# Kernel optimization log

Measured on AMD Instinct MI355X. Metric: run time of the kernel, lower is better.

Reference implementation:

```python
import jax, jax.numpy as jnp
import numpy as np

B, L, D_IN = 4, 2048, 1024
D_KEY, D_VAL = 1024, 1024
N_SLOTS, TOPK = 32768, 16
TEMP = 0.1
EPS = 1e-5


def layer_norm(x, g, b):
    mu = jnp.mean(x, axis=-1, keepdims=True)
    var = jnp.var(x, axis=-1, keepdims=True)
    return (x - mu) * jax.lax.rsqrt(var + EPS) * g + b


def setup_inputs() -> dict:
    key = jax.random.key(0)
    ks = jax.random.split(key, 8)
    s_in = 1.0 / np.sqrt(D_IN)
    s_ft = 1.0 / np.sqrt(D_IN + D_VAL + 1)
    return {
        "h_in": jax.random.normal(ks[0], (B, L, D_IN), jnp.float32),
        "Wk": jax.random.normal(ks[1], (D_IN, D_KEY), jnp.float32) * s_in,
        "bk": jnp.zeros((D_KEY,), jnp.float32),
        "cube_keys": jax.random.normal(ks[2], (N_SLOTS, D_KEY), jnp.float32),
        "cube_vals": jax.random.normal(ks[3], (N_SLOTS, D_VAL), jnp.float32) * 0.1,
        "ln_in_g": jnp.ones((D_IN,), jnp.float32),
        "ln_in_b": jnp.zeros((D_IN,), jnp.float32),
        "ln_pred_g": jnp.ones((D_VAL,), jnp.float32),
        "ln_pred_b": jnp.zeros((D_VAL,), jnp.float32),
        "W1": jax.random.normal(ks[4], (D_IN + D_VAL + 1, D_IN), jnp.float32) * s_ft,
        "b1": jnp.zeros((D_IN,), jnp.float32),
        "W2": jax.random.normal(ks[5], (D_IN, 1), jnp.float32) * s_in,
        "b2": jnp.zeros((1,), jnp.float32),
    }


def reference(h_in, Wk, bk, cube_keys, cube_vals, ln_in_g, ln_in_b,
              ln_pred_g, ln_pred_b, W1, b1, W2, b2):
    Bv, Lv, Dv = h_in.shape
    # key projection -> [B*L, d_key]
    keys = (jnp.einsum('bld,dk->blk', h_in, Wk) + bk).reshape(Bv * Lv, -1)
    # cube kNN query: cosine similarity against slot keys
    kn = keys * jax.lax.rsqrt(jnp.sum(keys * keys, -1, keepdims=True) + 1e-8)
    mn = cube_keys * jax.lax.rsqrt(jnp.sum(cube_keys * cube_keys, -1, keepdims=True) + 1e-8)
    sims = kn @ mn.T                                   # [BL, N]
    top_sims, idx = jax.lax.top_k(sims, TOPK)          # [BL, K]
    w = jax.nn.softmax(top_sims / TEMP, axis=-1)       # retrieval weights
    vals = jnp.take(cube_vals, idx, axis=0)            # [BL, K, d_val] gather
    pred = jnp.einsum('nk,nkd->nd', w, vals).reshape(Bv, Lv, -1)
    conf = ((top_sims[:, 0] + 1.0) * 0.5).reshape(Bv, Lv, 1)
    # gate
    feats = jnp.concatenate([layer_norm(h_in, ln_in_g, ln_in_b),
                             layer_norm(pred, ln_pred_g, ln_pred_b),
                             conf], axis=-1)
    hmid = jax.nn.silu(jnp.einsum('blf,fd->bld', feats, W1) + b1)
    alpha = jnp.clip(jax.nn.sigmoid(jnp.einsum('bld,do->blo', hmid, W2) + b2), 0.0, 1.0)
    # blend (y_teacher is None): (1-a)*h + a*(h+pred)
    y_out = (1.0 - alpha) * h_in + alpha * (h_in + pred)
    return y_out, jnp.mean(alpha), jnp.mean(conf)
```

## Files before the change

kernel.cpp:

```cpp
#include <hip/hip_runtime.h>
#include <hip/hip_bf16.h>
#include <cstdint>
#include <cstddef>

typedef __bf16 bf16;
typedef __bf16 bf16x4 __attribute__((ext_vector_type(4)));
typedef __bf16 bf16x8 __attribute__((ext_vector_type(8)));
typedef float  f32x4  __attribute__((ext_vector_type(4)));

#define BL      8192
#define DDIM    1024
#define NSLOTS  32768
#define NSPLIT  8
#define SLOTS_PER (NSLOTS / NSPLIT)
#define CAP     49

#define WS_MN    ((size_t)0)
#define WS_PRED  ((size_t)0)
#define WS_HBF   ((size_t)67108864)
#define WS_HMID  WS_HBF
#define WS_WKT   ((size_t)83886080)
#define WS_W1T   ((size_t)85983232)
#define WS_KEYS  ((size_t)90177536)
#define WS_FEATS WS_KEYS
#define WS_KN    ((size_t)123731968)
#define WS_TPK   ((size_t)140509184)
#define WS_CONF  ((size_t)148897792)

__device__ __forceinline__ void async16(const void* g, void* l) {
  __builtin_amdgcn_global_load_lds(
      (const __attribute__((address_space(1))) void*)g,
      (__attribute__((address_space(3))) void*)(uintptr_t)(uint32_t)(uintptr_t)l,
      16, 0, 0);
}

__device__ __forceinline__ void stage_tile(const bf16* __restrict__ src, int ld,
                                           bf16* lds, int tid) {
  const int wave = tid >> 6;
#pragma unroll
  for (int issue = 0; issue < 2; ++issue) {
    const int gi  = issue * 256 + tid;
    const int row = gi >> 2;
    const int gc  = gi & 3;
    const bf16* g = src + (size_t)row * ld + gc * 8;
    bf16* l = lds + (size_t)(issue * 256 + wave * 64) * 8;
    async16(g, l);
  }
}

__device__ __forceinline__ f32x4 mfma_bf16(bf16x8 a, bf16x8 b, f32x4 c) {
  return __builtin_amdgcn_mfma_f32_16x16x32_bf16(a, b, c, 0, 0, 0);
}

__device__ __forceinline__ float block_sum(float v, float* red) {
#pragma unroll
  for (int off = 32; off > 0; off >>= 1) v += __shfl_xor(v, off, 64);
  const int tid = threadIdx.x;
  if ((tid & 63) == 0) red[tid >> 6] = v;
  __syncthreads();
  v = red[0] + red[1] + red[2] + red[3];
  __syncthreads();
  return v;
}

__device__ __forceinline__ uint32_t pack_key(float v, int slot) {
  return ((__float_as_uint(v) ^ 0x80000000u) & 0xFFFF8000u) | (uint32_t)slot;
}

__device__ __forceinline__ void drain_merge(uint32_t* cand, int* cnt, int rb_own,
                                            uint32_t (&tk)[16], float& thrF) {
  int n = cnt[rb_own];
  n = n > CAP ? CAP : n;
  for (int t = 0;; ++t) {
    if (!__any(t < n)) break;
    uint32_t cur = 0u;
    if (t < n) cur = cand[rb_own * CAP + t];
#pragma unroll
    for (int p = 0; p < 16; ++p) {
      const uint32_t old = tk[p];
      const uint32_t mx = old > cur ? old : cur;
      tk[p] = mx;
      cur = old > cur ? cur : old;
    }
  }
  cnt[rb_own] = 0;
  thrF = __uint_as_float((tk[15] & 0xFFFF8000u) ^ 0x80000000u);
}

__global__ void cvt_bf16_kernel(const float* __restrict__ in, bf16* __restrict__ out, int n4) {
  int i = blockIdx.x * blockDim.x + threadIdx.x;
  if (i >= n4) return;
  f32x4 v = *(const f32x4*)(in + (size_t)i * 4);
  bf16x4 o = {(bf16)v.x, (bf16)v.y, (bf16)v.z, (bf16)v.w};
  *(bf16x4*)(out + (size_t)i * 4) = o;
}

__global__ void transpose_f32_bf16(const float* __restrict__ in, bf16* __restrict__ out,
                                   int R, int C) {
  __shared__ float tile[32][33];
  const int c0 = blockIdx.x * 32, r0 = blockIdx.y * 32;
  for (int i = threadIdx.y; i < 32; i += 8)
    tile[i][threadIdx.x] = in[(size_t)(r0 + i) * C + c0 + threadIdx.x];
  __syncthreads();
  for (int i = threadIdx.y; i < 32; i += 8)
    out[(size_t)(c0 + i) * R + r0 + threadIdx.x] = (bf16)tile[threadIdx.x][i];
}

__global__ __launch_bounds__(256) void rownorm_kernel(const float* __restrict__ in,
                                                      bf16* __restrict__ out) {
  __shared__ float red[4];
  const int row = blockIdx.x, t = threadIdx.x;
  f32x4 v = *(const f32x4*)(in + (size_t)row * 1024 + t * 4);
  float sq = v.x * v.x + v.y * v.y + v.z * v.z + v.w * v.w;
  sq = block_sum(sq, red);
  float sc = rsqrtf(sq + 1e-8f);
  bf16x4 o = {(bf16)(v.x * sc), (bf16)(v.y * sc), (bf16)(v.z * sc), (bf16)(v.w * sc)};
  *(bf16x4*)(out + (size_t)row * 1024 + t * 4) = o;
}

template <int EPI>
__global__ __launch_bounds__(256, 2) void gemm_bt_kernel(
    const bf16* __restrict__ A, const bf16* __restrict__ Bm, int Kd,
    float* __restrict__ Cf, bf16* __restrict__ Cb,
    const float* __restrict__ bias, const float* __restrict__ conf,
    const float* __restrict__ w1c) {
  __shared__ bf16 As[128 * 32];
  __shared__ bf16 Bs[128 * 32];
  const int tid = threadIdx.x;
  const int lane = tid & 63, wave = tid >> 6;
  const int wr = (wave >> 1) * 64, wc = (wave & 1) * 64;
  const int m0 = blockIdx.x * 128, n0 = blockIdx.y * 128;
  const int ar = lane & 15, ak = (lane >> 4) * 8;

  f32x4 acc[4][4];
#pragma unroll
  for (int i = 0; i < 4; ++i)
#pragma unroll
    for (int j = 0; j < 4; ++j) acc[i][j] = (f32x4){0.f, 0.f, 0.f, 0.f};

  for (int k0 = 0; k0 < Kd; k0 += 32) {
    __syncthreads();
    stage_tile(A + (size_t)m0 * Kd + k0, Kd, As, tid);
    stage_tile(Bm + (size_t)n0 * Kd + k0, Kd, Bs, tid);
    __syncthreads();
    bf16x8 af[4], bfr[4];
#pragma unroll
    for (int i = 0; i < 4; ++i)
      af[i] = *(const bf16x8*)(As + (wr + i * 16 + ar) * 32 + ak);
#pragma unroll
    for (int j = 0; j < 4; ++j)
      bfr[j] = *(const bf16x8*)(Bs + (wc + j * 16 + ar) * 32 + ak);
#pragma unroll
    for (int i = 0; i < 4; ++i)
#pragma unroll
      for (int j = 0; j < 4; ++j)
        acc[i][j] = mfma_bf16(af[i], bfr[j], acc[i][j]);
  }

  const int mq = (lane >> 4) * 4, nq = lane & 15;
#pragma unroll
  for (int i = 0; i < 4; ++i)
#pragma unroll
    for (int j = 0; j < 4; ++j)
#pragma unroll
      for (int r = 0; r < 4; ++r) {
        const int m = m0 + wr + i * 16 + mq + r;
        const int n = n0 + wc + j * 16 + nq;
        float x = acc[i][j][r];
        if (EPI == 0) {
          Cf[(size_t)m * 1024 + n] = x + bias[n];
        } else {
          x += bias[n] + conf[m] * w1c[n];
          x = x / (1.f + expf(-x));
          Cb[(size_t)m * 1024 + n] = (bf16)x;
        }
      }
}

__global__ __launch_bounds__(256, 2) void sims_topk_kernel(
    const bf16* __restrict__ kn, const bf16* __restrict__ mn,
    uint32_t* __restrict__ tpk) {
  __shared__ bf16 As[128 * 32];
  __shared__ bf16 Bs0[128 * 32];
  __shared__ bf16 Bs1[128 * 32];
  __shared__ uint32_t cand[256 * CAP];
  __shared__ int cnt[256];

  const int tid = threadIdx.x;
  const int lane = tid & 63, wave = tid >> 6;
  const int wr = (wave >> 1) * 64;
  const int ch = wave & 1;
  const int split = blockIdx.x;
  const int m0 = blockIdx.y * 128;
  const int sbeg = split * SLOTS_PER;
  const int ar = lane & 15, ak = (lane >> 4) * 8;
  const int mq = (lane >> 4) * 4, nq = lane & 15;
  const int rb_own = (wr + lane) * 2 + ch;

  cnt[tid] = 0;

  uint32_t tk[16];
#pragma unroll
  for (int j = 0; j < 16; ++j) tk[j] = 0u;
  float thrF = __uint_as_float(0x80000000u);

  for (int it = 0; it < SLOTS_PER / 256; ++it) {
    f32x4 acc[2][4][4];
#pragma unroll
    for (int c = 0; c < 2; ++c)
#pragma unroll
      for (int i = 0; i < 4; ++i)
#pragma unroll
        for (int j = 0; j < 4; ++j) acc[c][i][j] = (f32x4){0.f, 0.f, 0.f, 0.f};

    const int n0 = sbeg + it * 256;
    for (int k0 = 0; k0 < 1024; k0 += 32) {
      __syncthreads();
      stage_tile(kn + (size_t)m0 * 1024 + k0, 1024, As, tid);
      stage_tile(mn + (size_t)n0 * 1024 + k0, 1024, Bs0, tid);
      stage_tile(mn + (size_t)(n0 + 128) * 1024 + k0, 1024, Bs1, tid);
      __syncthreads();
      bf16x8 af[4], b0[4], b1[4];
#pragma unroll
      for (int i = 0; i < 4; ++i)
        af[i] = *(const bf16x8*)(As + (wr + i * 16 + ar) * 32 + ak);
#pragma unroll
      for (int j = 0; j < 4; ++j) {
        b0[j] = *(const bf16x8*)(Bs0 + (ch * 64 + j * 16 + ar) * 32 + ak);
        b1[j] = *(const bf16x8*)(Bs1 + (ch * 64 + j * 16 + ar) * 32 + ak);
      }
#pragma unroll
      for (int i = 0; i < 4; ++i)
#pragma unroll
        for (int j = 0; j < 4; ++j) {
          acc[0][i][j] = mfma_bf16(af[i], b0[j], acc[0][i][j]);
          acc[1][i][j] = mfma_bf16(af[i], b1[j], acc[1][i][j]);
        }
    }

#pragma unroll
    for (int cc = 0; cc < 2; ++cc) {
      const int colbase = sbeg + it * 256 + cc * 128 + ch * 64;
      uint64_t skip = 0ull;
#pragma unroll
      for (int i = 0; i < 4; ++i)
#pragma unroll
        for (int r = 0; r < 4; ++r) {
          const int owner = i * 16 + mq + r;
          const float thr = __shfl(thrF, owner, 64);
          const int rb = (wr + owner) * 2 + ch;
#pragma unroll
          for (int j = 0; j < 4; ++j) {
            const float v = acc[cc][i][j][r];
            if (v > thr) {
              const int old = atomicAdd(&cnt[rb], 1);
              if (old < CAP) cand[rb * CAP + old] = pack_key(v, colbase + j * 16 + nq);
              else skip |= (1ull << (i * 16 + r * 4 + j));
            }
          }
        }
      drain_merge(cand, cnt, rb_own, tk, thrF);
      if (__any(skip != 0ull)) {
#pragma unroll
        for (int i = 0; i < 4; ++i)
#pragma unroll
          for (int r = 0; r < 4; ++r) {
            const int owner = i * 16 + mq + r;
            const float thr = __shfl(thrF, owner, 64);
            const int rb = (wr + owner) * 2 + ch;
#pragma unroll
            for (int j = 0; j < 4; ++j) {
              if (skip & (1ull << (i * 16 + r * 4 + j))) {
                const float v = acc[cc][i][j][r];
                if (v > thr) {
                  const int old = atomicAdd(&cnt[rb], 1);
                  if (old < CAP) cand[rb * CAP + old] = pack_key(v, colbase + j * 16 + nq);
                }
              }
            }
          }
        drain_merge(cand, cnt, rb_own, tk, thrF);
      }
    }
  }

  const int row = m0 + wr + lane;
  uint32_t* dst = tpk + (((size_t)row * NSPLIT + split) * 2 + ch) * 16;
#pragma unroll
  for (int j = 0; j < 16; ++j) dst[j] = tk[j];
}

__global__ __launch_bounds__(256) void merge_pred_kernel(
    const uint32_t* __restrict__ tpk, const float* __restrict__ vals,
    float* __restrict__ pred, float* __restrict__ conf) {
  __shared__ uint32_t ks[256];
  __shared__ float sv[16];
  __shared__ int si[16];
  __shared__ float sw[16];
  const int row = blockIdx.x, t = threadIdx.x;
  const uint32_t k = tpk[(size_t)row * 256 + t];
  ks[t] = k;
  __syncthreads();
  int rank = 0;
  for (int j = 0; j < 256; ++j) rank += (ks[j] > k);
  if (rank < 16) {
    sv[rank] = __uint_as_float((k & 0xFFFF8000u) ^ 0x80000000u);
    si[rank] = (int)(k & 0x7FFFu);
  }
  __syncthreads();
  if (t == 0) {
    const float m = sv[0];
    float s = 0.f;
#pragma unroll
    for (int q = 0; q < 16; ++q) {
      float e = expf((sv[q] - m) * 10.f);
      sw[q] = e;
      s += e;
    }
    const float inv = 1.f / s;
#pragma unroll
    for (int q = 0; q < 16; ++q) sw[q] *= inv;
    conf[row] = (m + 1.f) * 0.5f;
  }
  __syncthreads();
  const int col = t * 4;
  f32x4 a = (f32x4){0.f, 0.f, 0.f, 0.f};
#pragma unroll
  for (int q = 0; q < 16; ++q) {
    f32x4 vv = *(const f32x4*)(vals + (size_t)si[q] * 1024 + col);
    a += vv * sw[q];
  }
  *(f32x4*)(pred + (size_t)row * 1024 + col) = a;
}

__global__ __launch_bounds__(256) void feats_kernel(
    const float* __restrict__ h, const float* __restrict__ pred,
    const float* __restrict__ gin, const float* __restrict__ bin,
    const float* __restrict__ gpr, const float* __restrict__ bpr,
    bf16* __restrict__ feats) {
  __shared__ float red[4];
  const int row = blockIdx.x, t = threadIdx.x;
  {
    f32x4 v = *(const f32x4*)(h + (size_t)row * 1024 + t * 4);
    float s = v.x + v.y + v.z + v.w;
    float sq = v.x * v.x + v.y * v.y + v.z * v.z + v.w * v.w;
    s = block_sum(s, red);
    sq = block_sum(sq, red);
    const float mean = s * (1.f / 1024.f);
    const float rstd = rsqrtf(sq * (1.f / 1024.f) - mean * mean + 1e-5f);
    f32x4 g = *(const f32x4*)(gin + t * 4);
    f32x4 b = *(const f32x4*)(bin + t * 4);
    bf16x4 o = {(bf16)((v.x - mean) * rstd * g.x + b.x),
                (bf16)((v.y - mean) * rstd * g.y + b.y),
                (bf16)((v.z - mean) * rstd * g.z + b.z),
                (bf16)((v.w - mean) * rstd * g.w + b.w)};
    *(bf16x4*)(feats + (size_t)row * 2048 + t * 4) = o;
  }
  {
    f32x4 v = *(const f32x4*)(pred + (size_t)row * 1024 + t * 4);
    float s = v.x + v.y + v.z + v.w;
    float sq = v.x * v.x + v.y * v.y + v.z * v.z + v.w * v.w;
    s = block_sum(s, red);
    sq = block_sum(sq, red);
    const float mean = s * (1.f / 1024.f);
    const float rstd = rsqrtf(sq * (1.f / 1024.f) - mean * mean + 1e-5f);
    f32x4 g = *(const f32x4*)(gpr + t * 4);
    f32x4 b = *(const f32x4*)(bpr + t * 4);
    bf16x4 o = {(bf16)((v.x - mean) * rstd * g.x + b.x),
                (bf16)((v.y - mean) * rstd * g.y + b.y),
                (bf16)((v.z - mean) * rstd * g.z + b.z),
                (bf16)((v.w - mean) * rstd * g.w + b.w)};
    *(bf16x4*)(feats + (size_t)row * 2048 + 1024 + t * 4) = o;
  }
}

__global__ __launch_bounds__(256) void final_kernel(
    const bf16* __restrict__ hmid, const float* __restrict__ W2,
    const float* __restrict__ b2, const float* __restrict__ h,
    const float* __restrict__ pred, const float* __restrict__ conf,
    float* __restrict__ out) {
  __shared__ float red[4];
  const int row = blockIdx.x, t = threadIdx.x;
  float s = 0.f;
#pragma unroll
  for (int j = 0; j < 4; ++j) {
    const int c = t + 256 * j;
    s += (float)hmid[(size_t)row * 1024 + c] * W2[c];
  }
  s = block_sum(s, red);
  float alpha = 1.f / (1.f + expf(-(s + b2[0])));
  alpha = fminf(fmaxf(alpha, 0.f), 1.f);
  f32x4 hv = *(const f32x4*)(h + (size_t)row * 1024 + t * 4);
  f32x4 pv = *(const f32x4*)(pred + (size_t)row * 1024 + t * 4);
  f32x4 y = hv + pv * alpha;
  *(f32x4*)(out + (size_t)row * 1024 + t * 4) = y;
  if (t == 0) {
    atomicAdd(out + 8388608, alpha * (1.f / 8192.f));
    atomicAdd(out + 8388609, conf[row] * (1.f / 8192.f));
  }
}

extern "C" void kernel_launch(void* const* d_in, const int* in_sizes, int n_in,
                              void* d_out, int out_size, void* d_ws, size_t ws_size,
                              hipStream_t stream) {
  const float* h_in      = (const float*)d_in[0];
  const float* Wk        = (const float*)d_in[1];
  const float* bk        = (const float*)d_in[2];
  const float* cube_keys = (const float*)d_in[3];
  const float* cube_vals = (const float*)d_in[4];
  const float* ln_in_g   = (const float*)d_in[5];
  const float* ln_in_b   = (const float*)d_in[6];
  const float* ln_pred_g = (const float*)d_in[7];
  const float* ln_pred_b = (const float*)d_in[8];
  const float* W1        = (const float*)d_in[9];
  const float* b1        = (const float*)d_in[10];
  const float* W2        = (const float*)d_in[11];
  const float* b2        = (const float*)d_in[12];

  char* ws = (char*)d_ws;
  bf16*     mn    = (bf16*)(ws + WS_MN);
  float*    pred  = (float*)(ws + WS_PRED);
  bf16*     h_bf  = (bf16*)(ws + WS_HBF);
  bf16*     hmid  = (bf16*)(ws + WS_HMID);
  bf16*     wkT   = (bf16*)(ws + WS_WKT);
  bf16*     w1T   = (bf16*)(ws + WS_W1T);
  float*    keys  = (float*)(ws + WS_KEYS);
  bf16*     feats = (bf16*)(ws + WS_FEATS);
  bf16*     kn    = (bf16*)(ws + WS_KN);
  uint32_t* tpk   = (uint32_t*)(ws + WS_TPK);
  float*    conf  = (float*)(ws + WS_CONF);
  float*    out   = (float*)d_out;
  const float* w1c = W1 + (size_t)2048 * 1024;

  cvt_bf16_kernel<<<(BL * DDIM / 4 + 255) / 256, 256, 0, stream>>>(h_in, h_bf, BL * DDIM / 4);
  transpose_f32_bf16<<<dim3(32, 32), dim3(32, 8), 0, stream>>>(Wk, wkT, 1024, 1024);
  transpose_f32_bf16<<<dim3(32, 64), dim3(32, 8), 0, stream>>>(W1, w1T, 2048, 1024);
  rownorm_kernel<<<NSLOTS, 256, 0, stream>>>(cube_keys, mn);

  gemm_bt_kernel<0><<<dim3(64, 8), 256, 0, stream>>>(h_bf, wkT, 1024, keys, nullptr,
                                                     bk, nullptr, nullptr);
  rownorm_kernel<<<BL, 256, 0, stream>>>(keys, kn);

  sims_topk_kernel<<<dim3(NSPLIT, 64), 256, 0, stream>>>(kn, mn, tpk);

  merge_pred_kernel<<<BL, 256, 0, stream>>>(tpk, cube_vals, pred, conf);

  feats_kernel<<<BL, 256, 0, stream>>>(h_in, pred, ln_in_g, ln_in_b,
                                       ln_pred_g, ln_pred_b, feats);
  gemm_bt_kernel<1><<<dim3(64, 8), 256, 0, stream>>>(feats, w1T, 2048, nullptr, hmid,
                                                     b1, conf, w1c);

  hipMemsetAsync(out + 8388608, 0, 8, stream);
  final_kernel<<<BL, 256, 0, stream>>>(hmid, W2, b2, h_in, pred, conf, out);
}
```

Baseline: 1.460 ms.

## Double-buffer LDS tiles with async prefetch in GEMM and sims-topk kernels

Both the GEMM and the fused similarity/top-k kernels now keep two LDS tile buffers and issue the next k-slice's async global-to-LDS loads before computing the current one. Explicit vmcnt/lgkmcnt waits and raw barriers replace the old pair of syncthreads around each load. The sims kernel's nested loops are flattened into one 512-step pipelined loop so prefetch carries across slot-block boundaries. The candidate buffer is shrunk from 49 to 17 per row, with the overflow retry turned into a loop, to free LDS for the extra buffers. The cost is more retry passes when many candidates pass the threshold.

```diff
diff --git a/kernel.cpp b/kernel.cpp
--- a/kernel.cpp
+++ b/kernel.cpp
@@ -13,7 +13,7 @@
 #define NSLOTS  32768
 #define NSPLIT  8
 #define SLOTS_PER (NSLOTS / NSPLIT)
-#define CAP     49
+#define CAP     17
 
 #define WS_MN    ((size_t)0)
 #define WS_PRED  ((size_t)0)
@@ -124,8 +124,8 @@
     float* __restrict__ Cf, bf16* __restrict__ Cb,
     const float* __restrict__ bias, const float* __restrict__ conf,
     const float* __restrict__ w1c) {
-  __shared__ bf16 As[128 * 32];
-  __shared__ bf16 Bs[128 * 32];
+  __shared__ bf16 As[2][128 * 32];
+  __shared__ bf16 Bs[2][128 * 32];
   const int tid = threadIdx.x;
   const int lane = tid & 63, wave = tid >> 6;
   const int wr = (wave >> 1) * 64, wc = (wave & 1) * 64;
@@ -138,23 +138,37 @@
 #pragma unroll
     for (int j = 0; j < 4; ++j) acc[i][j] = (f32x4){0.f, 0.f, 0.f, 0.f};
 
-  for (int k0 = 0; k0 < Kd; k0 += 32) {
-    __syncthreads();
-    stage_tile(A + (size_t)m0 * Kd + k0, Kd, As, tid);
-    stage_tile(Bm + (size_t)n0 * Kd + k0, Kd, Bs, tid);
-    __syncthreads();
+  const int NT = Kd >> 5;
+  stage_tile(A + (size_t)m0 * Kd, Kd, &As[0][0], tid);
+  stage_tile(Bm + (size_t)n0 * Kd, Kd, &Bs[0][0], tid);
+
+  for (int T = 0; T < NT; ++T) {
+    const int cur = T & 1;
+    if (T + 1 < NT) {
+      stage_tile(A + (size_t)m0 * Kd + (T + 1) * 32, Kd, &As[cur ^ 1][0], tid);
+      stage_tile(Bm + (size_t)n0 * Kd + (T + 1) * 32, Kd, &Bs[cur ^ 1][0], tid);
+      asm volatile("s_waitcnt vmcnt(4)" ::: "memory");
+    } else {
+      asm volatile("s_waitcnt vmcnt(0)" ::: "memory");
+    }
+    __builtin_amdgcn_s_barrier();
+    __builtin_amdgcn_sched_barrier(0);
+    const bf16* Ab = &As[cur][0];
+    const bf16* Bb = &Bs[cur][0];
     bf16x8 af[4], bfr[4];
 #pragma unroll
     for (int i = 0; i < 4; ++i)
-      af[i] = *(const bf16x8*)(As + (wr + i * 16 + ar) * 32 + ak);
+      af[i] = *(const bf16x8*)(Ab + (wr + i * 16 + ar) * 32 + ak);
 #pragma unroll
     for (int j = 0; j < 4; ++j)
-      bfr[j] = *(const bf16x8*)(Bs + (wc + j * 16 + ar) * 32 + ak);
+      bfr[j] = *(const bf16x8*)(Bb + (wc + j * 16 + ar) * 32 + ak);
 #pragma unroll
     for (int i = 0; i < 4; ++i)
 #pragma unroll
       for (int j = 0; j < 4; ++j)
         acc[i][j] = mfma_bf16(af[i], bfr[j], acc[i][j]);
+    asm volatile("s_waitcnt lgkmcnt(0)" ::: "memory");
+    __builtin_amdgcn_s_barrier();
   }
 
   const int mq = (lane >> 4) * 4, nq = lane & 15;
@@ -180,9 +194,9 @@
 __global__ __launch_bounds__(256, 2) void sims_topk_kernel(
     const bf16* __restrict__ kn, const bf16* __restrict__ mn,
     uint32_t* __restrict__ tpk) {
-  __shared__ bf16 As[128 * 32];
-  __shared__ bf16 Bs0[128 * 32];
-  __shared__ bf16 Bs1[128 * 32];
+  __shared__ bf16 As[2][128 * 32];
+  __shared__ bf16 Bs0[2][128 * 32];
+  __shared__ bf16 Bs1[2][128 * 32];
   __shared__ uint32_t cand[256 * CAP];
   __shared__ int cnt[256];
 
@@ -204,63 +218,66 @@
   for (int j = 0; j < 16; ++j) tk[j] = 0u;
   float thrF = __uint_as_float(0x80000000u);
 
-  for (int it = 0; it < SLOTS_PER / 256; ++it) {
-    f32x4 acc[2][4][4];
-#pragma unroll
-    for (int c = 0; c < 2; ++c)
-#pragma unroll
-      for (int i = 0; i < 4; ++i)
-#pragma unroll
-        for (int j = 0; j < 4; ++j) acc[c][i][j] = (f32x4){0.f, 0.f, 0.f, 0.f};
-
-    const int n0 = sbeg + it * 256;
-    for (int k0 = 0; k0 < 1024; k0 += 32) {
-      __syncthreads();
-      stage_tile(kn + (size_t)m0 * 1024 + k0, 1024, As, tid);
-      stage_tile(mn + (size_t)n0 * 1024 + k0, 1024, Bs0, tid);
-      stage_tile(mn + (size_t)(n0 + 128) * 1024 + k0, 1024, Bs1, tid);
-      __syncthreads();
-      bf16x8 af[4], b0[4], b1[4];
-#pragma unroll
-      for (int i = 0; i < 4; ++i)
-        af[i] = *(const bf16x8*)(As + (wr + i * 16 + ar) * 32 + ak);
+  f32x4 acc[2][4][4];
+
+  auto stage3 = [&](int Tt, int b) {
+    const int k0 = (Tt & 31) * 32;
+    const int n0 = sbeg + (Tt >> 5) * 256;
+    stage_tile(kn + (size_t)m0 * 1024 + k0, 1024, &As[b][0], tid);
+    stage_tile(mn + (size_t)n0 * 1024 + k0, 1024, &Bs0[b][0], tid);
+    stage_tile(mn + (size_t)(n0 + 128) * 1024 + k0, 1024, &Bs1[b][0], tid);
+  };
+
+  stage3(0, 0);
+
+  for (int T = 0; T < 512; ++T) {
+    const int cur = T & 1;
+    if ((T & 31) == 0) {
+#pragma unroll
+      for (int c = 0; c < 2; ++c)
+#pragma unroll
+        for (int i = 0; i < 4; ++i)
+#pragma unroll
+          for (int j = 0; j < 4; ++j) acc[c][i][j] = (f32x4){0.f, 0.f, 0.f, 0.f};
+    }
+
+    if (T + 1 < 512) {
+      stage3(T + 1, cur ^ 1);
+      asm volatile("s_waitcnt vmcnt(6)" ::: "memory");
+    } else {
+      asm volatile("s_waitcnt vmcnt(0)" ::: "memory");
+    }
+    __builtin_amdgcn_s_barrier();
+    __builtin_amdgcn_sched_barrier(0);
+
+    const bf16* Ab  = &As[cur][0];
+    const bf16* B0b = &Bs0[cur][0];
+    const bf16* B1b = &Bs1[cur][0];
+    bf16x8 af[4], b0[4], b1[4];
+#pragma unroll
+    for (int i = 0; i < 4; ++i)
+      af[i] = *(const bf16x8*)(Ab + (wr + i * 16 + ar) * 32 + ak);
+#pragma unroll
+    for (int j = 0; j < 4; ++j) {
+      b0[j] = *(const bf16x8*)(B0b + (ch * 64 + j * 16 + ar) * 32 + ak);
+      b1[j] = *(const bf16x8*)(B1b + (ch * 64 + j * 16 + ar) * 32 + ak);
+    }
+#pragma unroll
+    for (int i = 0; i < 4; ++i)
 #pragma unroll
       for (int j = 0; j < 4; ++j) {
-        b0[j] = *(const bf16x8*)(Bs0 + (ch * 64 + j * 16 + ar) * 32 + ak);
-        b1[j] = *(const bf16x8*)(Bs1 + (ch * 64 + j * 16 + ar) * 32 + ak);
+        acc[0][i][j] = mfma_bf16(af[i], b0[j], acc[0][i][j]);
+        acc[1][i][j] = mfma_bf16(af[i], b1[j], acc[1][i][j]);
       }
-#pragma unroll
-      for (int i = 0; i < 4; ++i)
-#pragma unroll
-        for (int j = 0; j < 4; ++j) {
-          acc[0][i][j] = mfma_bf16(af[i], b0[j], acc[0][i][j]);
-          acc[1][i][j] = mfma_bf16(af[i], b1[j], acc[1][i][j]);
-        }
-    }
-
-#pragma unroll
-    for (int cc = 0; cc < 2; ++cc) {
-      const int colbase = sbeg + it * 256 + cc * 128 + ch * 64;
-      uint64_t skip = 0ull;
-#pragma unroll
-      for (int i = 0; i < 4; ++i)
-#pragma unroll
-        for (int r = 0; r < 4; ++r) {
-          const int owner = i * 16 + mq + r;
-          const float thr = __shfl(thrF, owner, 64);
-          const int rb = (wr + owner) * 2 + ch;
-#pragma unroll
-          for (int j = 0; j < 4; ++j) {
-            const float v = acc[cc][i][j][r];
-            if (v > thr) {
-              const int old = atomicAdd(&cnt[rb], 1);
-              if (old < CAP) cand[rb * CAP + old] = pack_key(v, colbase + j * 16 + nq);
-              else skip |= (1ull << (i * 16 + r * 4 + j));
-            }
-          }
-        }
-      drain_merge(cand, cnt, rb_own, tk, thrF);
-      if (__any(skip != 0ull)) {
+    asm volatile("s_waitcnt lgkmcnt(0)" ::: "memory");
+    __builtin_amdgcn_s_barrier();
+
+    if ((T & 31) == 31) {
+      const int itn0 = sbeg + (T >> 5) * 256;
+#pragma unroll
+      for (int cc = 0; cc < 2; ++cc) {
+        const int colbase = itn0 + cc * 128 + ch * 64;
+        uint64_t skip = 0ull;
 #pragma unroll
         for (int i = 0; i < 4; ++i)
 #pragma unroll
@@ -270,16 +287,39 @@
             const int rb = (wr + owner) * 2 + ch;
 #pragma unroll
             for (int j = 0; j < 4; ++j) {
-              if (skip & (1ull << (i * 16 + r * 4 + j))) {
-                const float v = acc[cc][i][j][r];
-                if (v > thr) {
-                  const int old = atomicAdd(&cnt[rb], 1);
-                  if (old < CAP) cand[rb * CAP + old] = pack_key(v, colbase + j * 16 + nq);
-                }
+              const float v = acc[cc][i][j][r];
+              if (v > thr) {
+                const int old = atomicAdd(&cnt[rb], 1);
+                if (old < CAP) cand[rb * CAP + old] = pack_key(v, colbase + j * 16 + nq);
+                else skip |= (1ull << (i * 16 + r * 4 + j));
               }
             }
           }
         drain_merge(cand, cnt, rb_own, tk, thrF);
+        while (__any(skip != 0ull)) {
+          uint64_t ns = 0ull;
+#pragma unroll
+          for (int i = 0; i < 4; ++i)
+#pragma unroll
+            for (int r = 0; r < 4; ++r) {
+              const int owner = i * 16 + mq + r;
+              const float thr = __shfl(thrF, owner, 64);
+              const int rb = (wr + owner) * 2 + ch;
+#pragma unroll
+              for (int j = 0; j < 4; ++j) {
+                if (skip & (1ull << (i * 16 + r * 4 + j))) {
+                  const float v = acc[cc][i][j][r];
+                  if (v > thr) {
+                    const int old = atomicAdd(&cnt[rb], 1);
+                    if (old < CAP) cand[rb * CAP + old] = pack_key(v, colbase + j * 16 + nq);
+                    else ns |= (1ull << (i * 16 + r * 4 + j));
+                  }
+                }
+              }
+            }
+          drain_merge(cand, cnt, rb_own, tk, thrF);
+          skip = ns;
+        }
       }
     }
   }
```

After: 1.992 ms. +36.4%, slower.

## Double-buffer GEMM LDS tiles and XOR-swizzle tile layout to avoid bank conflicts

Applied to the files above, without the earlier changes.

The generic bf16 GEMM kernel now keeps two LDS buffers per operand, prefetching the next K-slice with async global-to-LDS loads while MFMAs run on the current one, synchronised with explicit vmcnt waits and barriers. Both the GEMM and the sims/top-k kernel switch to an XOR-swizzled column placement in the staging routine and matching read offsets, to cut LDS bank conflicts on fragment reads. Double buffering doubles the GEMM's LDS footprint, which may affect occupancy, and the hand-written waitcnt counts must match the number of outstanding loads.

```diff
diff --git a/kernel.cpp b/kernel.cpp
--- a/kernel.cpp
+++ b/kernel.cpp
@@ -41,7 +41,7 @@
   for (int issue = 0; issue < 2; ++issue) {
     const int gi  = issue * 256 + tid;
     const int row = gi >> 2;
-    const int gc  = gi & 3;
+    const int gc  = (gi & 3) ^ ((gi >> 3) & 3);
     const bf16* g = src + (size_t)row * ld + gc * 8;
     bf16* l = lds + (size_t)(issue * 256 + wave * 64) * 8;
     async16(g, l);
@@ -124,13 +124,16 @@
     float* __restrict__ Cf, bf16* __restrict__ Cb,
     const float* __restrict__ bias, const float* __restrict__ conf,
     const float* __restrict__ w1c) {
-  __shared__ bf16 As[128 * 32];
-  __shared__ bf16 Bs[128 * 32];
+  __shared__ bf16 As0[128 * 32];
+  __shared__ bf16 As1[128 * 32];
+  __shared__ bf16 Bs0[128 * 32];
+  __shared__ bf16 Bs1[128 * 32];
   const int tid = threadIdx.x;
   const int lane = tid & 63, wave = tid >> 6;
   const int wr = (wave >> 1) * 64, wc = (wave & 1) * 64;
   const int m0 = blockIdx.x * 128, n0 = blockIdx.y * 128;
-  const int ar = lane & 15, ak = (lane >> 4) * 8;
+  const int ar = lane & 15;
+  const int sw8 = (((lane >> 4) ^ ((ar >> 1) & 3)) << 3);
 
   f32x4 acc[4][4];
 #pragma unroll
@@ -138,23 +141,36 @@
 #pragma unroll
     for (int j = 0; j < 4; ++j) acc[i][j] = (f32x4){0.f, 0.f, 0.f, 0.f};
 
-  for (int k0 = 0; k0 < Kd; k0 += 32) {
-    __syncthreads();
-    stage_tile(A + (size_t)m0 * Kd + k0, Kd, As, tid);
-    stage_tile(Bm + (size_t)n0 * Kd + k0, Kd, Bs, tid);
-    __syncthreads();
+  const bf16 *Ac = As0, *An = As1, *Bc = Bs0, *Bn = Bs1;
+  const int NT = Kd >> 5;
+  stage_tile(A + (size_t)m0 * Kd, Kd, (bf16*)Ac, tid);
+  stage_tile(Bm + (size_t)n0 * Kd, Kd, (bf16*)Bc, tid);
+
+  for (int T = 0; T < NT; ++T) {
+    if (T + 1 < NT) {
+      stage_tile(A + (size_t)m0 * Kd + (T + 1) * 32, Kd, (bf16*)An, tid);
+      stage_tile(Bm + (size_t)n0 * Kd + (T + 1) * 32, Kd, (bf16*)Bn, tid);
+      asm volatile("s_waitcnt vmcnt(4)" ::: "memory");
+    } else {
+      asm volatile("s_waitcnt vmcnt(0)" ::: "memory");
+    }
+    __builtin_amdgcn_s_barrier();
     bf16x8 af[4], bfr[4];
 #pragma unroll
     for (int i = 0; i < 4; ++i)
-      af[i] = *(const bf16x8*)(As + (wr + i * 16 + ar) * 32 + ak);
+      af[i] = *(const bf16x8*)(Ac + (wr + i * 16 + ar) * 32 + sw8);
 #pragma unroll
     for (int j = 0; j < 4; ++j)
-      bfr[j] = *(const bf16x8*)(Bs + (wc + j * 16 + ar) * 32 + ak);
+      bfr[j] = *(const bf16x8*)(Bc + (wc + j * 16 + ar) * 32 + sw8);
 #pragma unroll
     for (int i = 0; i < 4; ++i)
 #pragma unroll
       for (int j = 0; j < 4; ++j)
         acc[i][j] = mfma_bf16(af[i], bfr[j], acc[i][j]);
+    asm volatile("s_waitcnt lgkmcnt(0)" ::: "memory");
+    __builtin_amdgcn_s_barrier();
+    const bf16* t0 = Ac; Ac = An; An = t0;
+    const bf16* t1 = Bc; Bc = Bn; Bn = t1;
   }
 
   const int mq = (lane >> 4) * 4, nq = lane & 15;
@@ -193,7 +209,8 @@
   const int split = blockIdx.x;
   const int m0 = blockIdx.y * 128;
   const int sbeg = split * SLOTS_PER;
-  const int ar = lane & 15, ak = (lane >> 4) * 8;
+  const int ar = lane & 15;
+  const int sw8 = (((lane >> 4) ^ ((ar >> 1) & 3)) << 3);
   const int mq = (lane >> 4) * 4, nq = lane & 15;
   const int rb_own = (wr + lane) * 2 + ch;
 
@@ -223,11 +240,11 @@
       bf16x8 af[4], b0[4], b1[4];
 #pragma unroll
       for (int i = 0; i < 4; ++i)
-        af[i] = *(const bf16x8*)(As + (wr + i * 16 + ar) * 32 + ak);
+        af[i] = *(const bf16x8*)(As + (wr + i * 16 + ar) * 32 + sw8);
 #pragma unroll
       for (int j = 0; j < 4; ++j) {
-        b0[j] = *(const bf16x8*)(Bs0 + (ch * 64 + j * 16 + ar) * 32 + ak);
-        b1[j] = *(const bf16x8*)(Bs1 + (ch * 64 + j * 16 + ar) * 32 + ak);
+        b0[j] = *(const bf16x8*)(Bs0 + (ch * 64 + j * 16 + ar) * 32 + sw8);
+        b1[j] = *(const bf16x8*)(Bs1 + (ch * 64 + j * 16 + ar) * 32 + sw8);
       }
 #pragma unroll
       for (int i = 0; i < 4; ++i)
```

Result: faster. 1.406 ms (-3.7%).
